# Kernel tuning notes

Measured on AMD Instinct MI355X. Metric: run time of the kernel, lower is better.

## Reference

```python
import jax, jax.numpy as jnp
import numpy as np

# static config (matches init_kwargs)
E = 1280          # n_embed
L = 4             # n_layer
NH = 16           # n_heads
D = E // NH       # head_dim = 80
M = 5120          # n_mlp
O = 2048          # n_output_embed
MS = 2            # spatial_merge_size
NGPS = 48         # sqrt(num_position_embeddings)
GRID_T, GRID_H, GRID_W = 1, 32, 32
N_IMG = 2
SPP = GRID_T * GRID_H * GRID_W   # 1024 tokens per image
S = N_IMG * SPP                  # 2048 total tokens
H4 = E * MS * MS                 # merger hidden = 5120
IN_PATCH = 3 * 2 * 16 * 16       # 1536
DS_IDX = [1, 2]


def _ln(x, w, b, eps=1e-6):
    m = x.mean(-1, keepdims=True)
    v = ((x - m) ** 2).mean(-1, keepdims=True)
    return (x - m) / jnp.sqrt(v + eps) * w + b


def _pos_embed_interp(pos_emb):
    # bilinear interpolation of the 48x48 learned grid to GRID_HxGRID_W, per image
    hi = jnp.linspace(0.0, NGPS - 1.0, GRID_H)
    wi = jnp.linspace(0.0, NGPS - 1.0, GRID_W)
    hf = hi.astype(jnp.int32); wf = wi.astype(jnp.int32)
    hc = jnp.minimum(hf + 1, NGPS - 1); wc = jnp.minimum(wf + 1, NGPS - 1)
    dh = hi - hf; dw = wi - wf
    idx = [(hf[:, None] * NGPS + wf[None]).ravel(), (hf[:, None] * NGPS + wc[None]).ravel(),
           (hc[:, None] * NGPS + wf[None]).ravel(), (hc[:, None] * NGPS + wc[None]).ravel()]
    wts = [((1 - dh)[:, None] * (1 - dw)[None]).ravel(), ((1 - dh)[:, None] * dw[None]).ravel(),
           (dh[:, None] * (1 - dw)[None]).ravel(), (dh[:, None] * dw[None]).ravel()]
    pe = sum(pos_emb[i] * w[:, None] for i, w in zip(idx, wts))  # [h*w, E]
    pe = jnp.tile(pe, (GRID_T, 1))
    # spatial-merge permutation: (t, h/m, m, w/m, m) -> (t, h/m, w/m, m, m)
    pe = pe.reshape(GRID_T, GRID_H // MS, MS, GRID_W // MS, MS, E).transpose(0, 1, 3, 2, 4, 5).reshape(-1, E)
    return jnp.tile(pe, (N_IMG, 1))  # [S, E]


def _rotary_freqs():
    dim = D // 2  # VisionRotaryEmbedding dim = 40
    inv = 1.0 / (10000.0 ** (jnp.arange(0, dim, 2, dtype=jnp.float32) / dim))  # [D//4]
    hp = jnp.broadcast_to(jnp.arange(GRID_H)[:, None], (GRID_H, GRID_W))
    hp = hp.reshape(GRID_H // MS, MS, GRID_W // MS, MS).transpose(0, 2, 1, 3).ravel()
    wp = jnp.broadcast_to(jnp.arange(GRID_W)[None, :], (GRID_H, GRID_W))
    wp = wp.reshape(GRID_H // MS, MS, GRID_W // MS, MS).transpose(0, 2, 1, 3).ravel()
    pos = jnp.stack([hp, wp], -1)            # [h*w, 2]
    pos = jnp.tile(pos, (GRID_T, 1))
    pos = jnp.tile(pos, (N_IMG, 1))          # [S, 2]
    table = jnp.arange(max(GRID_H, GRID_W), dtype=jnp.float32)[:, None] * inv[None]  # [G, D//4]
    return table[pos].reshape(S, -1)         # [S, D//2] (h-freqs || w-freqs)


def _rope(t, cos, sin):
    # t: [S, NH, D]; cos/sin: [S, 1, D]; applied in float32 as in the source
    t1, t2 = jnp.split(t, 2, axis=-1)
    rot = jnp.concatenate([-t2, t1], -1)
    return (t.astype(jnp.float32) * cos + rot.astype(jnp.float32) * sin).astype(t.dtype)


def _attn(x, qkv_w, qkv_b, pw, pb, cos, sin, mask):
    qkv = (x @ qkv_w.T + qkv_b).reshape(S, 3, NH, D)
    q, k, v = qkv[:, 0], qkv[:, 1], qkv[:, 2]
    q = _rope(q, cos, sin)
    k = _rope(k, cos, sin)
    scores = jnp.einsum('shd,thd->hst', q, k) / np.sqrt(D).astype(np.float32) + mask
    p = jax.nn.softmax(scores.astype(jnp.float32), axis=-1).astype(q.dtype)
    o = jnp.einsum('hst,thd->shd', p, v).reshape(S, E)
    return o @ pw.T + pb


def _merger(x, ln_w, ln_b, f1w, f1b, f2w, f2b, post):
    if post:
        x = _ln(x.reshape(-1, H4), ln_w, ln_b)
    else:
        x = _ln(x, ln_w, ln_b).reshape(-1, H4)
    h = jax.nn.gelu(x @ f1w.T + f1b, approximate=False)  # nn.GELU() exact
    return h @ f2w.T + f2b


def setup_inputs() -> dict:
    key = jax.random.key(0)
    ks = iter(jax.random.split(key, 24))
    n = lambda s: jax.random.normal(next(ks), s, dtype=jnp.float32) * 0.02
    return {
        'x': jax.random.normal(next(ks), (S, IN_PATCH), dtype=jnp.float32),
        'patch_w': n((E, IN_PATCH)), 'patch_b': jnp.zeros((E,), jnp.float32),
        'pos_emb': n((NGPS * NGPS, E)),
        'ln1_w': jnp.ones((L, E), jnp.float32), 'ln1_b': jnp.zeros((L, E), jnp.float32),
        'ln2_w': jnp.ones((L, E), jnp.float32), 'ln2_b': jnp.zeros((L, E), jnp.float32),
        'qkv_w': n((L, 3 * E, E)), 'qkv_b': jnp.zeros((L, 3 * E), jnp.float32),
        'attn_proj_w': n((L, E, E)), 'attn_proj_b': jnp.zeros((L, E), jnp.float32),
        'fc1_w': n((L, M, E)), 'fc1_b': jnp.zeros((L, M), jnp.float32),
        'fc2_w': n((L, E, M)), 'fc2_b': jnp.zeros((L, E), jnp.float32),
        'm_ln_w': jnp.ones((E,), jnp.float32), 'm_ln_b': jnp.zeros((E,), jnp.float32),
        'm_fc1_w': n((H4, H4)), 'm_fc1_b': jnp.zeros((H4,), jnp.float32),
        'm_fc2_w': n((O, H4)), 'm_fc2_b': jnp.zeros((O,), jnp.float32),
        'ds_ln_w': jnp.ones((2, H4), jnp.float32), 'ds_ln_b': jnp.zeros((2, H4), jnp.float32),
        'ds_fc1_w': n((2, H4, H4)), 'ds_fc1_b': jnp.zeros((2, H4), jnp.float32),
        'ds_fc2_w': n((2, O, H4)), 'ds_fc2_b': jnp.zeros((2, O), jnp.float32),
    }


def reference(x, patch_w, patch_b, pos_emb, ln1_w, ln1_b, ln2_w, ln2_b,
              qkv_w, qkv_b, attn_proj_w, attn_proj_b, fc1_w, fc1_b, fc2_w, fc2_b,
              m_ln_w, m_ln_b, m_fc1_w, m_fc1_b, m_fc2_w, m_fc2_b,
              ds_ln_w, ds_ln_b, ds_fc1_w, ds_fc1_b, ds_fc2_w, ds_fc2_b):
    # patch embed (Conv3d with kernel==stride == per-patch linear)
    h = x @ patch_w.T + patch_b                      # [S, E]
    h = h + _pos_embed_interp(pos_emb)
    freqs = _rotary_freqs()                          # [S, D//2]
    cos = jnp.concatenate([jnp.cos(freqs)] * 2, -1)[:, None, :]  # [S,1,D]
    sin = jnp.concatenate([jnp.sin(freqs)] * 2, -1)[:, None, :]
    img = jnp.arange(S) // SPP                       # cu_seqlens block-diagonal mask
    mask = jnp.where(img[:, None] == img[None, :], 0.0, jnp.finfo(jnp.float32).min)
    ds_feats = []
    for l in range(L):
        h = h + _attn(_ln(h, ln1_w[l], ln1_b[l]), qkv_w[l], qkv_b[l],
                      attn_proj_w[l], attn_proj_b[l], cos, sin, mask)
        hn = _ln(h, ln2_w[l], ln2_b[l])
        h = h + (jax.nn.gelu(hn @ fc1_w[l].T + fc1_b[l], approximate=True) @ fc2_w[l].T + fc2_b[l])
        if l in DS_IDX:
            j = DS_IDX.index(l)
            ds_feats.append(_merger(h, ds_ln_w[j], ds_ln_b[j], ds_fc1_w[j], ds_fc1_b[j],
                                    ds_fc2_w[j], ds_fc2_b[j], post=True))
    main = _merger(h, m_ln_w, m_ln_b, m_fc1_w, m_fc1_b, m_fc2_w, m_fc2_b, post=False)
    return jnp.stack([main] + ds_feats, 0)           # [3, S//4, O]
```

## Files before the change

kernel.cpp:

```cpp
#include <hip/hip_runtime.h>
#include <hip/hip_bf16.h>
#include <cstdio>
#include <cstdint>

#define E_    1280
#define L_    4
#define NH_   16
#define D_    80
#define DP_   96
#define MLP_  5120
#define O_    2048
#define S_    2048
#define H4_   5120
#define INP_  1536

typedef __attribute__((ext_vector_type(4))) float f32x4;
typedef __attribute__((ext_vector_type(8))) short short8v;
typedef __attribute__((ext_vector_type(4))) short short4v;

__device__ __forceinline__ short f2bf(float f){
  uint32_t u = __float_as_uint(f);
  uint32_t r = (u + 0x7FFFu + ((u >> 16) & 1u)) >> 16;
  return (short)r;
}
__device__ __forceinline__ float bf2f(short s){
  return __uint_as_float(((uint32_t)(uint16_t)s) << 16);
}
__device__ __forceinline__ float gelu_tanh(float x){
  const float z = 0.7978845608028654f*(x + 0.044715f*x*x*x);
  const float e = __expf(2.f*z);
  return 0.5f*x*(1.f + (e-1.f)/(e+1.f));
}
__device__ __forceinline__ float gelu_erf(float x){
  return 0.5f*x*(1.f + erff(x*0.7071067811865476f));
}
__device__ __forceinline__ void token_hw(int t, int& hc, int& wc){
  hc = ((t>>1)&1) + ((t>>6)<<1);
  wc = (t&1)      + (((t>>2)&15)<<1);
}
__device__ __forceinline__ void gload16(const short* g, short* l){
  __builtin_amdgcn_global_load_lds((const __attribute__((address_space(1))) void*)g,
                                   (__attribute__((address_space(3))) void*)l, 16, 0, 0);
}

__global__ __launch_bounds__(256)
void cvt_k(const float* __restrict__ src, short* __restrict__ dst, long long n)
{
  const long long stride = (long long)gridDim.x*256*8;
  for (long long i = ((long long)blockIdx.x*256 + threadIdx.x)*8; i < n; i += stride){
    float4 v0 = *(const float4*)(src+i);
    float4 v1 = *(const float4*)(src+i+4);
    short8v w;
    w[0]=f2bf(v0.x); w[1]=f2bf(v0.y); w[2]=f2bf(v0.z); w[3]=f2bf(v0.w);
    w[4]=f2bf(v1.x); w[5]=f2bf(v1.y); w[6]=f2bf(v1.z); w[7]=f2bf(v1.w);
    *(short8v*)(dst+i) = w;
  }
}

struct Gemm2P {
  const short* A; const short* B; void* C;
  const float* bias;
  short* part;
  int lda, ldb, ldc, M, N, K;
  float scale;
  long long aOffH, aOffI, bOffH, bOffI, cOffH, cOffI;
  int nImg, kSplit;
};

template<int EPI, bool RES, bool CF32, bool SPLIT>
__global__ __launch_bounds__(256)
void gemm2_k(Gemm2P p)
{
  __shared__ short As[3][4096];
  __shared__ short Bs[3][4096];

  int z = blockIdx.z, ks = 0;
  if constexpr (SPLIT){ ks = z % p.kSplit; z /= p.kSplit; }
  const int hI = z / p.nImg, iI = z % p.nImg;
  const long long aB = (long long)hI*p.aOffH + (long long)iI*p.aOffI;
  const long long bB = (long long)hI*p.bOffH + (long long)iI*p.bOffI;
  const long long cB = (long long)hI*p.cOffH + (long long)iI*p.cOffI;

  const int nwg = gridDim.x*gridDim.y;
  const int orig = blockIdx.y*gridDim.x + blockIdx.x;
  const int q8 = nwg >> 3, r8 = nwg & 7;
  const int xcd = orig & 7, oidx = orig >> 3;
  const int wg = (xcd < r8 ? xcd*(q8+1) : r8*(q8+1) + (xcd-r8)*q8) + oidx;
  const int nt = wg % gridDim.x, mt = wg / gridDim.x;

  const int tid = threadIdx.x, lane = tid & 63, wv = tid >> 6;

  const int lam = lane ^ ((lane >> 3) & 7);
  const int sr = lam >> 2;
  const int sc = (lam & 3) * 8;
  const int Kp  = SPLIT ? p.K / p.kSplit : p.K;
  const int kBeg = SPLIT ? ks * Kp : 0;
  const short* pa0 = p.A + aB + (long long)(mt*128 + (wv*2+0)*16 + sr)*p.lda + sc + kBeg;
  const short* pa1 = p.A + aB + (long long)(mt*128 + (wv*2+1)*16 + sr)*p.lda + sc + kBeg;
  const short* pb0 = p.B + bB + (long long)(nt*128 + (wv*2+0)*16 + sr)*p.ldb + sc + kBeg;
  const short* pb1 = p.B + bB + (long long)(nt*128 + (wv*2+1)*16 + sr)*p.ldb + sc + kBeg;
  const int so0 = (wv*2+0)*512;
  const int so1 = (wv*2+1)*512;

  const int fr = lane & 15, g4 = lane >> 4;
  const int wr = (wv >> 1) * 64, wc = (wv & 1) * 64;

  f32x4 acc[4][4] = {};

  auto stage = [&](int buf, int t){
    const int k0 = t << 5;
    gload16(pa0 + k0, &As[buf][so0]);
    gload16(pa1 + k0, &As[buf][so1]);
    gload16(pb0 + k0, &Bs[buf][so0]);
    gload16(pb1 + k0, &Bs[buf][so1]);
  };

  const int ntile = Kp >> 5;
  stage(0, 0);
  if (ntile > 1) stage(1, 1);
  for (int t = 0; t < ntile; t++){
    const int cur = t % 3;
    if (t + 1 < ntile) { asm volatile("s_waitcnt vmcnt(4)" ::: "memory"); }
    else               { asm volatile("s_waitcnt vmcnt(0)" ::: "memory"); }
    __builtin_amdgcn_s_barrier();
    asm volatile("" ::: "memory");
    short8v a[4], b[4];
    #pragma unroll
    for (int i=0;i<4;i++){
      const int ra = wr + i*16 + fr;
      const int ca = (ra*4 + g4) ^ ((ra>>1)&7);
      a[i] = *(const short8v*)&As[cur][ca*8];
      const int rb = wc + i*16 + fr;
      const int cb = (rb*4 + g4) ^ ((rb>>1)&7);
      b[i] = *(const short8v*)&Bs[cur][cb*8];
    }
    if (t + 2 < ntile) stage((t+2)%3, t+2);
    #pragma unroll
    for (int i=0;i<4;i++)
      #pragma unroll
      for (int j=0;j<4;j++)
        acc[i][j] = __builtin_amdgcn_mfma_f32_16x16x32_bf16(a[i], b[j], acc[i][j], 0, 0, 0);
  }

  #pragma unroll
  for (int i=0;i<4;i++){
    #pragma unroll
    for (int j=0;j<4;j++){
      #pragma unroll
      for (int r=0;r<4;r++){
        const int row = mt*128 + wr + i*16 + g4*4 + r;
        const int col = nt*128 + wc + j*16 + fr;
        float v = acc[i][j][r];
        if constexpr (SPLIT){
          p.part[((long long)ks*p.M + row)*p.N + col] = f2bf(v);
        } else {
          if (p.bias) v += p.bias[col];
          if constexpr (EPI==1) v = gelu_tanh(v);
          if constexpr (EPI==2) v = gelu_erf(v);
          if constexpr (EPI==3) v *= p.scale;
          const long long off = cB + (long long)row*p.ldc + col;
          if constexpr (RES)  v += ((const float*)p.C)[off];
          if constexpr (CF32) ((float*)p.C)[off] = v;
          else                ((short*)p.C)[off] = f2bf(v);
        }
      }
    }
  }
}

template<int EPI, bool RES, bool CF32>
__global__ __launch_bounds__(256)
void reduce_k(const short* __restrict__ part, int kSplit, long long MN, int N,
              const float* __restrict__ bias, void* __restrict__ C)
{
  const long long i = ((long long)blockIdx.x*256 + threadIdx.x)*8;
  if (i >= MN) return;
  float v[8];
  { short8v pv = *(const short8v*)(part + i);
    #pragma unroll
    for (int e=0;e<8;e++) v[e] = bf2f(pv[e]); }
  for (int ks = 1; ks < kSplit; ks++){
    short8v pv = *(const short8v*)(part + (long long)ks*MN + i);
    #pragma unroll
    for (int e=0;e<8;e++) v[e] += bf2f(pv[e]);
  }
  if (bias){
    const int col = (int)(i % N);
    #pragma unroll
    for (int e=0;e<8;e++) v[e] += bias[col+e];
  }
  #pragma unroll
  for (int e=0;e<8;e++){
    if constexpr (EPI==1) v[e] = gelu_tanh(v[e]);
    if constexpr (EPI==2) v[e] = gelu_erf(v[e]);
  }
  if constexpr (RES){
    const float* cp = (const float*)C + i;
    #pragma unroll
    for (int e=0;e<8;e++) v[e] += cp[e];
  }
  if constexpr (CF32){
    float4 o0 = {v[0],v[1],v[2],v[3]}, o1 = {v[4],v[5],v[6],v[7]};
    *(float4*)((float*)C + i) = o0;
    *(float4*)((float*)C + i + 4) = o1;
  } else {
    short8v o;
    #pragma unroll
    for (int e=0;e<8;e++) o[e] = f2bf(v[e]);
    *(short8v*)((short*)C + i) = o;
  }
}

__global__ __launch_bounds__(256)
void redln_k(const short* __restrict__ part, long long MN, const float* __restrict__ bias,
             float* __restrict__ h, const float* __restrict__ lnw, const float* __restrict__ lnb,
             short* __restrict__ aln)
{
  __shared__ float red[8];
  const int row = blockIdx.x, tid = threadIdx.x;
  float4 vals[2];
  float s = 0.f, sq = 0.f;
  #pragma unroll
  for (int it=0; it<2; it++){
    const int c = tid*4 + it*1024;
    if (c < E_){
      float4 v = *(const float4*)(h + (long long)row*E_ + c);
      const float4 b = *(const float4*)(bias + c);
      v.x += b.x; v.y += b.y; v.z += b.z; v.w += b.w;
      #pragma unroll
      for (int ks=0; ks<4; ks++){
        short4v pv = *(const short4v*)(part + (long long)ks*MN + (long long)row*E_ + c);
        v.x += bf2f(pv[0]); v.y += bf2f(pv[1]); v.z += bf2f(pv[2]); v.w += bf2f(pv[3]);
      }
      *(float4*)(h + (long long)row*E_ + c) = v;
      vals[it] = v;
      s  += v.x+v.y+v.z+v.w;
      sq += v.x*v.x+v.y*v.y+v.z*v.z+v.w*v.w;
    }
  }
  #pragma unroll
  for (int m=32;m;m>>=1){ s += __shfl_xor(s,m,64); sq += __shfl_xor(sq,m,64); }
  const int wv = tid>>6, lane = tid&63;
  if (lane==0){ red[wv]=s; red[4+wv]=sq; }
  __syncthreads();
  s  = red[0]+red[1]+red[2]+red[3];
  sq = red[4]+red[5]+red[6]+red[7];
  const float mean = s / (float)E_;
  const float var  = sq / (float)E_ - mean*mean;
  const float rs   = rsqrtf(var + 1e-6f);
  #pragma unroll
  for (int it=0; it<2; it++){
    const int c = tid*4 + it*1024;
    if (c < E_){
      const float4 v = vals[it];
      const float4 gw = *(const float4*)(lnw + c);
      const float4 bw = *(const float4*)(lnb + c);
      short4v o;
      o[0] = f2bf((v.x-mean)*rs*gw.x + bw.x);
      o[1] = f2bf((v.y-mean)*rs*gw.y + bw.y);
      o[2] = f2bf((v.z-mean)*rs*gw.z + bw.z);
      o[3] = f2bf((v.w-mean)*rs*gw.w + bw.w);
      *(short4v*)(aln + (long long)row*E_ + c) = o;
    }
  }
}

__global__ __launch_bounds__(256)
void redposln_k(const short* __restrict__ part, long long MN, const float* __restrict__ bias,
                const float* __restrict__ pe, float* __restrict__ h,
                const float* __restrict__ lnw, const float* __restrict__ lnb,
                short* __restrict__ aln)
{
  __shared__ float red[8];
  const int row = blockIdx.x, tid = threadIdx.x;
  const int t = row & 1023;
  int hc, wc; token_hw(t, hc, wc);
  const float hi = (float)hc * (47.f/31.f);
  const float wi = (float)wc * (47.f/31.f);
  int hf = (int)hi; float dh = hi - (float)hf; int h2 = min(hf+1, 47);
  int wf = (int)wi; float dw = wi - (float)wf; int w2 = min(wf+1, 47);
  const float w00=(1.f-dh)*(1.f-dw), w01=(1.f-dh)*dw, w10=dh*(1.f-dw), w11=dh*dw;
  const float* pe00 = pe + (long long)(hf*48+wf)*E_;
  const float* pe01 = pe + (long long)(hf*48+w2)*E_;
  const float* pe10 = pe + (long long)(h2*48+wf)*E_;
  const float* pe11 = pe + (long long)(h2*48+w2)*E_;

  float4 vals[2];
  float s = 0.f, sq = 0.f;
  #pragma unroll
  for (int it=0; it<2; it++){
    const int c = tid*4 + it*1024;
    if (c < E_){
      const float4 b = *(const float4*)(bias + c);
      const float4 a0 = *(const float4*)(pe00 + c);
      const float4 a1 = *(const float4*)(pe01 + c);
      const float4 a2 = *(const float4*)(pe10 + c);
      const float4 a3 = *(const float4*)(pe11 + c);
      float4 v;
      v.x = b.x + w00*a0.x + w01*a1.x + w10*a2.x + w11*a3.x;
      v.y = b.y + w00*a0.y + w01*a1.y + w10*a2.y + w11*a3.y;
      v.z = b.z + w00*a0.z + w01*a1.z + w10*a2.z + w11*a3.z;
      v.w = b.w + w00*a0.w + w01*a1.w + w10*a2.w + w11*a3.w;
      #pragma unroll
      for (int ks=0; ks<4; ks++){
        short4v pv = *(const short4v*)(part + (long long)ks*MN + (long long)row*E_ + c);
        v.x += bf2f(pv[0]); v.y += bf2f(pv[1]); v.z += bf2f(pv[2]); v.w += bf2f(pv[3]);
      }
      *(float4*)(h + (long long)row*E_ + c) = v;
      vals[it] = v;
      s  += v.x+v.y+v.z+v.w;
      sq += v.x*v.x+v.y*v.y+v.z*v.z+v.w*v.w;
    }
  }
  #pragma unroll
  for (int m=32;m;m>>=1){ s += __shfl_xor(s,m,64); sq += __shfl_xor(sq,m,64); }
  const int wv = tid>>6, lane = tid&63;
  if (lane==0){ red[wv]=s; red[4+wv]=sq; }
  __syncthreads();
  s  = red[0]+red[1]+red[2]+red[3];
  sq = red[4]+red[5]+red[6]+red[7];
  const float mean = s / (float)E_;
  const float var  = sq / (float)E_ - mean*mean;
  const float rs   = rsqrtf(var + 1e-6f);
  #pragma unroll
  for (int it=0; it<2; it++){
    const int c = tid*4 + it*1024;
    if (c < E_){
      const float4 v = vals[it];
      const float4 gw = *(const float4*)(lnw + c);
      const float4 bw = *(const float4*)(lnb + c);
      short4v o;
      o[0] = f2bf((v.x-mean)*rs*gw.x + bw.x);
      o[1] = f2bf((v.y-mean)*rs*gw.y + bw.y);
      o[2] = f2bf((v.z-mean)*rs*gw.z + bw.z);
      o[3] = f2bf((v.w-mean)*rs*gw.w + bw.w);
      *(short4v*)(aln + (long long)row*E_ + c) = o;
    }
  }
}

__global__ __launch_bounds__(256)
void fattn_k(const short* __restrict__ qh, const short* __restrict__ kh,
             const short* __restrict__ vt, short* __restrict__ o2)
{
  __shared__ short Ps[4][16*136];

  const int qt = blockIdx.x, h = blockIdx.y, img = blockIdx.z;
  const int tid = threadIdx.x, lane = tid & 63, wv = tid >> 6;
  const int fr = lane & 15, fo = (lane >> 4) * 8, g = lane >> 4;

  const short* qp = qh + ((long long)h*S_ + img*1024 + qt*64 + wv*16)*DP_;
  const short* kp = kh + ((long long)h*S_ + img*1024)*DP_;
  const short* vp = vt + ((long long)(h*2 + img))*80*1024;
  short* Pw = &Ps[wv][0];

  short8v q[3];
  #pragma unroll
  for (int t3=0;t3<3;t3++)
    q[t3] = *(const short8v*)(qp + (long long)fr*DP_ + t3*32 + fo);

  float m_[4], l_[4];
  f32x4 ao[5] = {};
  #pragma unroll
  for (int r=0;r<4;r++){ m_[r] = -3.0e38f; l_[r] = 0.f; }

  const float SC = 0.11180339887498949f * 1.4426950408889634f;

  for (int t = 0; t < 8; t++){
    f32x4 sc[8] = {};
    #pragma unroll
    for (int j=0;j<8;j++){
      #pragma unroll
      for (int t3=0;t3<3;t3++){
        const short8v kb = *(const short8v*)(kp + (long long)(t*128 + j*16 + fr)*DP_ + t3*32 + fo);
        sc[j] = __builtin_amdgcn_mfma_f32_16x16x32_bf16(q[t3], kb, sc[j], 0,0,0);
      }
    }
    #pragma unroll
    for (int j=0;j<8;j++) sc[j] *= SC;

    #pragma unroll
    for (int r=0;r<4;r++){
      float mx = sc[0][r];
      #pragma unroll
      for (int j=1;j<8;j++) mx = fmaxf(mx, sc[j][r]);
      mx = fmaxf(mx, __shfl_xor(mx, 1, 64));
      mx = fmaxf(mx, __shfl_xor(mx, 2, 64));
      mx = fmaxf(mx, __shfl_xor(mx, 4, 64));
      mx = fmaxf(mx, __shfl_xor(mx, 8, 64));
      const float mn = fmaxf(m_[r], mx);
      const float al = exp2f(m_[r] - mn);
      float ts = 0.f;
      #pragma unroll
      for (int j=0;j<8;j++){
        const float pv = exp2f(sc[j][r] - mn);
        sc[j][r] = pv;
        ts += pv;
      }
      ts += __shfl_xor(ts, 1, 64);
      ts += __shfl_xor(ts, 2, 64);
      ts += __shfl_xor(ts, 4, 64);
      ts += __shfl_xor(ts, 8, 64);
      l_[r] = l_[r]*al + ts;
      m_[r] = mn;
      #pragma unroll
      for (int n=0;n<5;n++) ao[n][r] *= al;
      const int prow = g*4 + r;
      #pragma unroll
      for (int j=0;j<8;j++) Pw[prow*136 + j*16 + fr] = f2bf(sc[j][r]);
    }
    asm volatile("s_waitcnt lgkmcnt(0)" ::: "memory");
    __builtin_amdgcn_sched_barrier(0);

    #pragma unroll
    for (int t4=0;t4<4;t4++){
      const short8v pa = *(const short8v*)&Pw[fr*136 + t4*32 + fo];
      #pragma unroll
      for (int n=0;n<5;n++){
        const short8v vb = *(const short8v*)(vp + (long long)(n*16 + fr)*1024 + t*128 + t4*32 + fo);
        ao[n] = __builtin_amdgcn_mfma_f32_16x16x32_bf16(pa, vb, ao[n], 0,0,0);
      }
    }
  }

  short* op = o2 + ((long long)(img*1024 + qt*64 + wv*16))*E_ + h*80;
  #pragma unroll
  for (int r=0;r<4;r++){
    const float inv = 1.f / l_[r];
    const int row = g*4 + r;
    #pragma unroll
    for (int n=0;n<5;n++)
      op[(long long)row*E_ + n*16 + fr] = f2bf(ao[n][r] * inv);
  }
}

__global__ __launch_bounds__(256)
void ln_k(const float* __restrict__ X, const float* __restrict__ g, const float* __restrict__ bta,
          short* __restrict__ Y, int Cn)
{
  __shared__ float red[8];
  const int row = blockIdx.x;
  const float* x = X + (long long)row*Cn;
  short* y = Y + (long long)row*Cn;
  float s = 0.f, sq = 0.f;
  for (int c = threadIdx.x*4; c < Cn; c += 1024){
    float4 v = *(const float4*)(x + c);
    s  += v.x+v.y+v.z+v.w;
    sq += v.x*v.x+v.y*v.y+v.z*v.z+v.w*v.w;
  }
  #pragma unroll
  for (int m=32;m;m>>=1){ s += __shfl_xor(s,m,64); sq += __shfl_xor(sq,m,64); }
  const int wv = threadIdx.x>>6, lane = threadIdx.x&63;
  if (lane==0){ red[wv]=s; red[4+wv]=sq; }
  __syncthreads();
  s  = red[0]+red[1]+red[2]+red[3];
  sq = red[4]+red[5]+red[6]+red[7];
  const float mean = s / (float)Cn;
  const float var  = sq / (float)Cn - mean*mean;
  const float rs   = rsqrtf(var + 1e-6f);
  for (int c = threadIdx.x*4; c < Cn; c += 1024){
    float4 v  = *(const float4*)(x + c);
    float4 gw = *(const float4*)(g + c);
    float4 bw = *(const float4*)(bta + c);
    short4v o;
    o[0] = f2bf((v.x-mean)*rs*gw.x + bw.x);
    o[1] = f2bf((v.y-mean)*rs*gw.y + bw.y);
    o[2] = f2bf((v.z-mean)*rs*gw.z + bw.z);
    o[3] = f2bf((v.w-mean)*rs*gw.w + bw.w);
    *(short4v*)(y + c) = o;
  }
}

__global__ __launch_bounds__(256)
void rope_k(const short* __restrict__ qkv, short* __restrict__ qh,
            short* __restrict__ kh, short* __restrict__ vt)
{
  const int idx = blockIdx.x*256 + threadIdx.x;
  if (idx >= S_*NH_*40) return;
  const int d0 = idx % 40;
  const int h  = (idx / 40) % NH_;
  const int s  = idx / (40*NH_);
  const int t  = s & 1023, img = s >> 10;
  int hc, wc; token_hw(t, hc, wc);
  const int j  = d0 % 20;
  const float invf = exp2f(-0.66438561897747f * (float)j);
  const float pos  = (float)((d0 < 20) ? hc : wc);
  float sn, cs;
  __sincosf(pos * invf, &sn, &cs);
  const short* base = qkv + (long long)s*3840 + h*80;
  const float q1 = bf2f(base[d0]),      q2 = bf2f(base[d0+40]);
  const float k1 = bf2f(base[1280+d0]), k2 = bf2f(base[1280+d0+40]);
  const long long qo = ((long long)h*S_ + s)*DP_;
  qh[qo + d0]    = f2bf(q1*cs - q2*sn);
  qh[qo + d0+40] = f2bf(q2*cs + q1*sn);
  kh[qo + d0]    = f2bf(k1*cs - k2*sn);
  kh[qo + d0+40] = f2bf(k2*cs + k1*sn);
  if (d0 < 16){ qh[qo + 80 + d0] = 0; kh[qo + 80 + d0] = 0; }
  const long long vo = (((long long)h*2 + img)*80)*1024 + t;
  vt[vo + (long long)d0*1024]      = base[2560+d0];
  vt[vo + (long long)(d0+40)*1024] = base[2560+d0+40];
}

static Gemm2P mk(const short* A, const short* B, void* C, const float* bias,
                 int lda, int ldb, int ldc, int M, int N, int K, float scale = 1.f)
{
  Gemm2P p{}; p.A=A; p.B=B; p.C=C; p.bias=bias; p.part=nullptr;
  p.lda=lda; p.ldb=ldb; p.ldc=ldc; p.M=M; p.N=N; p.K=K; p.scale=scale;
  p.aOffH=p.aOffI=p.bOffH=p.bOffI=p.cOffH=p.cOffI=0; p.nImg=1; p.kSplit=1;
  return p;
}

extern "C" void kernel_launch(void* const* d_in, const int* in_sizes, int n_in,
                              void* d_out, int out_size, void* d_ws, size_t ws_size,
                              hipStream_t stream)
{
  const float* x           = (const float*)d_in[0];
  const float* patch_w     = (const float*)d_in[1];
  const float* patch_b     = (const float*)d_in[2];
  const float* pos_emb     = (const float*)d_in[3];
  const float* ln1_w       = (const float*)d_in[4];
  const float* ln1_b       = (const float*)d_in[5];
  const float* ln2_w       = (const float*)d_in[6];
  const float* ln2_b       = (const float*)d_in[7];
  const float* qkv_w       = (const float*)d_in[8];
  const float* qkv_b       = (const float*)d_in[9];
  const float* attn_proj_w = (const float*)d_in[10];
  const float* attn_proj_b = (const float*)d_in[11];
  const float* fc1_w       = (const float*)d_in[12];
  const float* fc1_b       = (const float*)d_in[13];
  const float* fc2_w       = (const float*)d_in[14];
  const float* fc2_b       = (const float*)d_in[15];
  const float* m_ln_w      = (const float*)d_in[16];
  const float* m_ln_b      = (const float*)d_in[17];
  const float* m_fc1_w     = (const float*)d_in[18];
  const float* m_fc1_b     = (const float*)d_in[19];
  const float* m_fc2_w     = (const float*)d_in[20];
  const float* m_fc2_b     = (const float*)d_in[21];
  const float* ds_ln_w     = (const float*)d_in[22];
  const float* ds_ln_b     = (const float*)d_in[23];
  const float* ds_fc1_w    = (const float*)d_in[24];
  const float* ds_fc1_b    = (const float*)d_in[25];
  const float* ds_fc2_w    = (const float*)d_in[26];
  const float* ds_fc2_b    = (const float*)d_in[27];
  float* out = (float*)d_out;

  char* wsp = (char*)d_ws;
  auto alloc = [&](size_t bytes)->char*{
    char* p = wsp; wsp += (bytes + 255) & ~(size_t)255; return p;
  };
  float* h    = (float*)alloc((size_t)S_*E_*4);
  short* qkvb = (short*)alloc((size_t)S_*3840*2);
  short* aln  = (short*)alloc((size_t)S_*E_*2);
  short* qh   = (short*)alloc((size_t)NH_*S_*DP_*2);
  short* kh   = (short*)alloc((size_t)NH_*S_*DP_*2 + 4096);
  short* vt   = (short*)alloc((size_t)NH_*2*D_*1024*2 + 4096);
  short* part = (short*)alloc((size_t)48*1024*1024);
  short* o2   = (short*)alloc((size_t)S_*E_*2);
  short* ffn  = (short*)alloc((size_t)S_*MLP_*2);
  short* xb    = (short*)alloc((size_t)S_*INP_*2);
  short* pwB   = (short*)alloc((size_t)E_*INP_*2);
  short* qkvwB = (short*)alloc((size_t)L_*3840*E_*2);
  short* prwB  = (short*)alloc((size_t)L_*E_*E_*2);
  short* f1wB  = (short*)alloc((size_t)L_*MLP_*E_*2);
  short* f2wB  = (short*)alloc((size_t)L_*E_*MLP_*2);
  short* mf1B  = (short*)alloc((size_t)H4_*H4_*2);
  short* mf2B  = (short*)alloc((size_t)O_*H4_*2);
  short* df1B  = (short*)alloc((size_t)2*H4_*H4_*2);
  short* df2B  = (short*)alloc((size_t)2*O_*H4_*2);
  size_t need = (size_t)(wsp - (char*)d_ws);
  if (need > ws_size){
    fprintf(stderr, "kernel_launch: ws too small: need %zu have %zu\n", need, ws_size);
    return;
  }
  short* dsln = qkvb;

  const dim3 B256(256);
  auto cvt = [&](const float* src, short* dst, long long n){
    unsigned blk = (unsigned)min((long long)8192, (n/8 + 255)/256);
    cvt_k<<<blk, B256, 0, stream>>>(src, dst, n);
  };
  cvt(x, xb, (long long)S_*INP_);
  cvt(patch_w, pwB, (long long)E_*INP_);
  cvt(qkv_w, qkvwB, (long long)L_*3840*E_);
  cvt(attn_proj_w, prwB, (long long)L_*E_*E_);
  cvt(fc1_w, f1wB, (long long)L_*MLP_*E_);
  cvt(fc2_w, f2wB, (long long)L_*E_*MLP_);
  cvt(m_fc1_w, mf1B, (long long)H4_*H4_);
  cvt(m_fc2_w, mf2B, (long long)O_*H4_);
  cvt(ds_fc1_w, df1B, (long long)2*H4_*H4_);
  cvt(ds_fc2_w, df2B, (long long)2*O_*H4_);

  auto G = [](int M, int N, int ks = 1){
    return dim3((unsigned)((N+127)/128), (unsigned)((M+127)/128), (unsigned)ks);
  };
  auto RG = [](long long MN){ return dim3((unsigned)((MN/8 + 255)/256)); };

  { Gemm2P pp = mk(xb, pwB, nullptr, nullptr, INP_, INP_, E_, S_, E_, INP_);
    pp.part = part; pp.kSplit = 4;
    gemm2_k<0,false,true,true><<<G(S_,E_,4),B256,0,stream>>>(pp);
    redposln_k<<<S_, B256, 0, stream>>>(part, (long long)S_*E_, patch_b, pos_emb,
                                        h, ln1_w, ln1_b, aln); }

  for (int l = 0; l < L_; l++){
    { Gemm2P pp = mk(aln, qkvwB + (size_t)l*3840*E_, qkvb, qkv_b + l*3840, E_, E_, 3840, S_, 3840, E_);
      gemm2_k<0,false,false,false><<<G(S_,3840),B256,0,stream>>>(pp); }
    rope_k<<<(S_*NH_*40+255)/256, B256, 0, stream>>>(qkvb, qh, kh, vt);
    fattn_k<<<dim3(16,16,2), B256, 0, stream>>>(qh, kh, vt, o2);
    { Gemm2P pp = mk(o2, prwB + (size_t)l*E_*E_, nullptr, nullptr, E_, E_, E_, S_, E_, E_);
      pp.part = part; pp.kSplit = 4;
      gemm2_k<0,false,true,true><<<G(S_,E_,4),B256,0,stream>>>(pp);
      redln_k<<<S_, B256, 0, stream>>>(part, (long long)S_*E_, attn_proj_b + l*E_,
                                       h, ln2_w + l*E_, ln2_b + l*E_, aln); }

    { Gemm2P pp = mk(aln, f1wB + (size_t)l*MLP_*E_, ffn, fc1_b + l*MLP_, E_, E_, MLP_, S_, MLP_, E_);
      gemm2_k<1,false,false,false><<<G(S_,MLP_),B256,0,stream>>>(pp); }
    { Gemm2P pp = mk(ffn, f2wB + (size_t)l*E_*MLP_, nullptr, nullptr, MLP_, MLP_, E_, S_, E_, MLP_);
      pp.part = part; pp.kSplit = 4;
      gemm2_k<0,false,true,true><<<G(S_,E_,4),B256,0,stream>>>(pp);
      const float* nw = (l < 3) ? (ln1_w + (l+1)*E_) : m_ln_w;
      const float* nb = (l < 3) ? (ln1_b + (l+1)*E_) : m_ln_b;
      redln_k<<<S_, B256, 0, stream>>>(part, (long long)S_*E_, fc2_b + l*E_, h, nw, nb, aln); }

    if (l == 1 || l == 2){
      const int j = l - 1;
      ln_k<<<512, B256, 0, stream>>>(h, ds_ln_w + (size_t)j*H4_, ds_ln_b + (size_t)j*H4_, dsln, H4_);
      { Gemm2P pp = mk(dsln, df1B + (size_t)j*H4_*H4_, ffn, nullptr, H4_, H4_, H4_, 512, H4_, H4_);
        pp.part = part; pp.kSplit = 4;
        gemm2_k<0,false,false,true><<<G(512,H4_,4),B256,0,stream>>>(pp);
        reduce_k<2,false,false><<<RG((long long)512*H4_),B256,0,stream>>>(part, 4, (long long)512*H4_, H4_, ds_fc1_b + (size_t)j*H4_, ffn); }
      { Gemm2P pp = mk(ffn, df2B + (size_t)j*O_*H4_, out + (size_t)(1+j)*512*O_, nullptr, H4_, H4_, O_, 512, O_, H4_);
        pp.part = part; pp.kSplit = 8;
        gemm2_k<0,false,true,true><<<G(512,O_,8),B256,0,stream>>>(pp);
        reduce_k<0,false,true><<<RG((long long)512*O_),B256,0,stream>>>(part, 8, (long long)512*O_, O_, ds_fc2_b + (size_t)j*O_, out + (size_t)(1+j)*512*O_); }
    }
  }

  { Gemm2P pp = mk(aln, mf1B, ffn, nullptr, H4_, H4_, H4_, 512, H4_, H4_);
    pp.part = part; pp.kSplit = 4;
    gemm2_k<0,false,false,true><<<G(512,H4_,4),B256,0,stream>>>(pp);
    reduce_k<2,false,false><<<RG((long long)512*H4_),B256,0,stream>>>(part, 4, (long long)512*H4_, H4_, m_fc1_b, ffn); }
  { Gemm2P pp = mk(ffn, mf2B, out, nullptr, H4_, H4_, O_, 512, O_, H4_);
    pp.part = part; pp.kSplit = 8;
    gemm2_k<0,false,true,true><<<G(512,O_,8),B256,0,stream>>>(pp);
    reduce_k<0,false,true><<<RG((long long)512*O_),B256,0,stream>>>(part, 8, (long long)512*O_, O_, m_fc2_b, out); }
}
```

Baseline: 1.647 ms.

## Fuse fp32-to-bf16 weight conversion into GEMM B-tile loading

Drops the separate conversion kernels that turned every fp32 weight matrix into bf16 before the GEMMs. The GEMM now loads fp32 B tiles into registers, converts them to bf16, and writes them to swizzled LDS one stage ahead, while A still uses direct global-to-LDS loads. This removes a full read and write pass over all weights per call, but doubles the bytes fetched for B inside each GEMM and adds register pressure and conversion ALU work to the main loop. It also removes unused batching and scale fields from the GEMM parameters.

```diff
diff --git a/kernel.cpp b/kernel.cpp
--- a/kernel.cpp
+++ b/kernel.cpp
@@ -58,13 +58,12 @@
 }
 
 struct Gemm2P {
-  const short* A; const short* B; void* C;
+  const short* A; const float* B; void* C;
   const float* bias;
   short* part;
   int lda, ldb, ldc, M, N, K;
   float scale;
-  long long aOffH, aOffI, bOffH, bOffI, cOffH, cOffI;
-  int nImg, kSplit;
+  int kSplit;
 };
 
 template<int EPI, bool RES, bool CF32, bool SPLIT>
@@ -74,12 +73,8 @@
   __shared__ short As[3][4096];
   __shared__ short Bs[3][4096];
 
-  int z = blockIdx.z, ks = 0;
-  if constexpr (SPLIT){ ks = z % p.kSplit; z /= p.kSplit; }
-  const int hI = z / p.nImg, iI = z % p.nImg;
-  const long long aB = (long long)hI*p.aOffH + (long long)iI*p.aOffI;
-  const long long bB = (long long)hI*p.bOffH + (long long)iI*p.bOffI;
-  const long long cB = (long long)hI*p.cOffH + (long long)iI*p.cOffI;
+  int ks = 0;
+  if constexpr (SPLIT){ ks = blockIdx.z; }
 
   const int nwg = gridDim.x*gridDim.y;
   const int orig = blockIdx.y*gridDim.x + blockIdx.x;
@@ -89,39 +84,65 @@
   const int nt = wg % gridDim.x, mt = wg / gridDim.x;
 
   const int tid = threadIdx.x, lane = tid & 63, wv = tid >> 6;
-
-  const int lam = lane ^ ((lane >> 3) & 7);
-  const int sr = lam >> 2;
-  const int sc = (lam & 3) * 8;
   const int Kp  = SPLIT ? p.K / p.kSplit : p.K;
   const int kBeg = SPLIT ? ks * Kp : 0;
-  const short* pa0 = p.A + aB + (long long)(mt*128 + (wv*2+0)*16 + sr)*p.lda + sc + kBeg;
-  const short* pa1 = p.A + aB + (long long)(mt*128 + (wv*2+1)*16 + sr)*p.lda + sc + kBeg;
-  const short* pb0 = p.B + bB + (long long)(nt*128 + (wv*2+0)*16 + sr)*p.ldb + sc + kBeg;
-  const short* pb1 = p.B + bB + (long long)(nt*128 + (wv*2+1)*16 + sr)*p.ldb + sc + kBeg;
+
+  const int lam = lane ^ ((lane >> 3) & 7);
+  const int asr = lam >> 2, asc = (lam & 3) * 8;
+  const short* pa0 = p.A + (long long)(mt*128 + (wv*2+0)*16 + asr)*p.lda + asc + kBeg;
+  const short* pa1 = p.A + (long long)(mt*128 + (wv*2+1)*16 + asr)*p.lda + asc + kBeg;
   const int so0 = (wv*2+0)*512;
   const int so1 = (wv*2+1)*512;
 
+  const int bsr = lane >> 2, bcc = lane & 3;
+  const int brow0 = (wv*2+0)*16 + bsr, brow1 = (wv*2+1)*16 + bsr;
+  const float* pbf0 = p.B + (long long)(nt*128 + brow0)*p.ldb + bcc*8 + kBeg;
+  const float* pbf1 = p.B + (long long)(nt*128 + brow1)*p.ldb + bcc*8 + kBeg;
+  const int wch0 = ((brow0*4 + bcc) ^ ((brow0>>1)&7)) * 8;
+  const int wch1 = ((brow1*4 + bcc) ^ ((brow1>>1)&7)) * 8;
+
   const int fr = lane & 15, g4 = lane >> 4;
   const int wr = (wv >> 1) * 64, wc = (wv & 1) * 64;
 
   f32x4 acc[4][4] = {};
-
-  auto stage = [&](int buf, int t){
+  float4 br0, br1, br2, br3;
+
+  auto loadB = [&](int t){
+    const int k0 = t << 5;
+    br0 = *(const float4*)(pbf0 + k0);
+    br1 = *(const float4*)(pbf0 + k0 + 4);
+    br2 = *(const float4*)(pbf1 + k0);
+    br3 = *(const float4*)(pbf1 + k0 + 4);
+  };
+  auto stageA = [&](int buf, int t){
     const int k0 = t << 5;
     gload16(pa0 + k0, &As[buf][so0]);
     gload16(pa1 + k0, &As[buf][so1]);
-    gload16(pb0 + k0, &Bs[buf][so0]);
-    gload16(pb1 + k0, &Bs[buf][so1]);
   };
+  auto writeB = [&](int buf){
+    short8v w0, w1;
+    w0[0]=f2bf(br0.x); w0[1]=f2bf(br0.y); w0[2]=f2bf(br0.z); w0[3]=f2bf(br0.w);
+    w0[4]=f2bf(br1.x); w0[5]=f2bf(br1.y); w0[6]=f2bf(br1.z); w0[7]=f2bf(br1.w);
+    w1[0]=f2bf(br2.x); w1[1]=f2bf(br2.y); w1[2]=f2bf(br2.z); w1[3]=f2bf(br2.w);
+    w1[4]=f2bf(br3.x); w1[5]=f2bf(br3.y); w1[6]=f2bf(br3.z); w1[7]=f2bf(br3.w);
+    *(short8v*)&Bs[buf][wch0] = w0;
+    *(short8v*)&Bs[buf][wch1] = w1;
+  };
 
   const int ntile = Kp >> 5;
-  stage(0, 0);
-  if (ntile > 1) stage(1, 1);
+  loadB(0);
+  stageA(0, 0);
+  asm volatile("s_waitcnt vmcnt(2)" ::: "memory");
+  writeB(0);
+  if (ntile > 1){ loadB(1); stageA(1, 1); }
+
   for (int t = 0; t < ntile; t++){
     const int cur = t % 3;
-    if (t + 1 < ntile) { asm volatile("s_waitcnt vmcnt(4)" ::: "memory"); }
+    if (t + 1 < ntile) { asm volatile("s_waitcnt vmcnt(2)" ::: "memory"); }
     else               { asm volatile("s_waitcnt vmcnt(0)" ::: "memory"); }
+    if (t + 1 < ntile) writeB((t+1) % 3);
+    if (t + 2 < ntile) loadB(t+2);
+    asm volatile("s_waitcnt lgkmcnt(0)" ::: "memory");
     __builtin_amdgcn_s_barrier();
     asm volatile("" ::: "memory");
     short8v a[4], b[4];
@@ -134,7 +155,7 @@
       const int cb = (rb*4 + g4) ^ ((rb>>1)&7);
       b[i] = *(const short8v*)&Bs[cur][cb*8];
     }
-    if (t + 2 < ntile) stage((t+2)%3, t+2);
+    if (t + 2 < ntile) stageA((t+2)%3, t+2);
     #pragma unroll
     for (int i=0;i<4;i++)
       #pragma unroll
@@ -157,8 +178,7 @@
           if (p.bias) v += p.bias[col];
           if constexpr (EPI==1) v = gelu_tanh(v);
           if constexpr (EPI==2) v = gelu_erf(v);
-          if constexpr (EPI==3) v *= p.scale;
-          const long long off = cB + (long long)row*p.ldc + col;
+          const long long off = (long long)row*p.ldc + col;
           if constexpr (RES)  v += ((const float*)p.C)[off];
           if constexpr (CF32) ((float*)p.C)[off] = v;
           else                ((short*)p.C)[off] = f2bf(v);
@@ -501,12 +521,11 @@
   vt[vo + (long long)(d0+40)*1024] = base[2560+d0+40];
 }
 
-static Gemm2P mk(const short* A, const short* B, void* C, const float* bias,
-                 int lda, int ldb, int ldc, int M, int N, int K, float scale = 1.f)
+static Gemm2P mk(const short* A, const float* B, void* C, const float* bias,
+                 int lda, int ldb, int ldc, int M, int N, int K)
 {
   Gemm2P p{}; p.A=A; p.B=B; p.C=C; p.bias=bias; p.part=nullptr;
-  p.lda=lda; p.ldb=ldb; p.ldc=ldc; p.M=M; p.N=N; p.K=K; p.scale=scale;
-  p.aOffH=p.aOffI=p.bOffH=p.bOffI=p.cOffH=p.cOffI=0; p.nImg=1; p.kSplit=1;
+  p.lda=lda; p.ldb=ldb; p.ldc=ldc; p.M=M; p.N=N; p.K=K; p.scale=1.f; p.kSplit=1;
   return p;
 }
 
@@ -557,16 +576,7 @@
   short* part = (short*)alloc((size_t)48*1024*1024);
   short* o2   = (short*)alloc((size_t)S_*E_*2);
   short* ffn  = (short*)alloc((size_t)S_*MLP_*2);
-  short* xb    = (short*)alloc((size_t)S_*INP_*2);
-  short* pwB   = (short*)alloc((size_t)E_*INP_*2);
-  short* qkvwB = (short*)alloc((size_t)L_*3840*E_*2);
-  short* prwB  = (short*)alloc((size_t)L_*E_*E_*2);
-  short* f1wB  = (short*)alloc((size_t)L_*MLP_*E_*2);
-  short* f2wB  = (short*)alloc((size_t)L_*E_*MLP_*2);
-  short* mf1B  = (short*)alloc((size_t)H4_*H4_*2);
-  short* mf2B  = (short*)alloc((size_t)O_*H4_*2);
-  short* df1B  = (short*)alloc((size_t)2*H4_*H4_*2);
-  short* df2B  = (short*)alloc((size_t)2*O_*H4_*2);
+  short* xb   = (short*)alloc((size_t)S_*INP_*2);
   size_t need = (size_t)(wsp - (char*)d_ws);
   if (need > ws_size){
     fprintf(stderr, "kernel_launch: ws too small: need %zu have %zu\n", need, ws_size);
@@ -575,46 +585,35 @@
   short* dsln = qkvb;
 
   const dim3 B256(256);
-  auto cvt = [&](const float* src, short* dst, long long n){
+  { long long n = (long long)S_*INP_;
     unsigned blk = (unsigned)min((long long)8192, (n/8 + 255)/256);
-    cvt_k<<<blk, B256, 0, stream>>>(src, dst, n);
-  };
-  cvt(x, xb, (long long)S_*INP_);
-  cvt(patch_w, pwB, (long long)E_*INP_);
-  cvt(qkv_w, qkvwB, (long long)L_*3840*E_);
-  cvt(attn_proj_w, prwB, (long long)L_*E_*E_);
-  cvt(fc1_w, f1wB, (long long)L_*MLP_*E_);
-  cvt(fc2_w, f2wB, (long long)L_*E_*MLP_);
-  cvt(m_fc1_w, mf1B, (long long)H4_*H4_);
-  cvt(m_fc2_w, mf2B, (long long)O_*H4_);
-  cvt(ds_fc1_w, df1B, (long long)2*H4_*H4_);
-  cvt(ds_fc2_w, df2B, (long long)2*O_*H4_);
+    cvt_k<<<blk, B256, 0, stream>>>(x, xb, n); }
 
   auto G = [](int M, int N, int ks = 1){
     return dim3((unsigned)((N+127)/128), (unsigned)((M+127)/128), (unsigned)ks);
   };
   auto RG = [](long long MN){ return dim3((unsigned)((MN/8 + 255)/256)); };
 
-  { Gemm2P pp = mk(xb, pwB, nullptr, nullptr, INP_, INP_, E_, S_, E_, INP_);
+  { Gemm2P pp = mk(xb, patch_w, nullptr, nullptr, INP_, INP_, E_, S_, E_, INP_);
     pp.part = part; pp.kSplit = 4;
     gemm2_k<0,false,true,true><<<G(S_,E_,4),B256,0,stream>>>(pp);
     redposln_k<<<S_, B256, 0, stream>>>(part, (long long)S_*E_, patch_b, pos_emb,
                                         h, ln1_w, ln1_b, aln); }
 
   for (int l = 0; l < L_; l++){
-    { Gemm2P pp = mk(aln, qkvwB + (size_t)l*3840*E_, qkvb, qkv_b + l*3840, E_, E_, 3840, S_, 3840, E_);
+    { Gemm2P pp = mk(aln, qkv_w + (size_t)l*3840*E_, qkvb, qkv_b + l*3840, E_, E_, 3840, S_, 3840, E_);
       gemm2_k<0,false,false,false><<<G(S_,3840),B256,0,stream>>>(pp); }
     rope_k<<<(S_*NH_*40+255)/256, B256, 0, stream>>>(qkvb, qh, kh, vt);
     fattn_k<<<dim3(16,16,2), B256, 0, stream>>>(qh, kh, vt, o2);
-    { Gemm2P pp = mk(o2, prwB + (size_t)l*E_*E_, nullptr, nullptr, E_, E_, E_, S_, E_, E_);
+    { Gemm2P pp = mk(o2, attn_proj_w + (size_t)l*E_*E_, nullptr, nullptr, E_, E_, E_, S_, E_, E_);
       pp.part = part; pp.kSplit = 4;
       gemm2_k<0,false,true,true><<<G(S_,E_,4),B256,0,stream>>>(pp);
       redln_k<<<S_, B256, 0, stream>>>(part, (long long)S_*E_, attn_proj_b + l*E_,
                                        h, ln2_w + l*E_, ln2_b + l*E_, aln); }
 
-    { Gemm2P pp = mk(aln, f1wB + (size_t)l*MLP_*E_, ffn, fc1_b + l*MLP_, E_, E_, MLP_, S_, MLP_, E_);
+    { Gemm2P pp = mk(aln, fc1_w + (size_t)l*MLP_*E_, ffn, fc1_b + l*MLP_, E_, E_, MLP_, S_, MLP_, E_);
       gemm2_k<1,false,false,false><<<G(S_,MLP_),B256,0,stream>>>(pp); }
-    { Gemm2P pp = mk(ffn, f2wB + (size_t)l*E_*MLP_, nullptr, nullptr, MLP_, MLP_, E_, S_, E_, MLP_);
+    { Gemm2P pp = mk(ffn, fc2_w + (size_t)l*E_*MLP_, nullptr, nullptr, MLP_, MLP_, E_, S_, E_, MLP_);
       pp.part = part; pp.kSplit = 4;
       gemm2_k<0,false,true,true><<<G(S_,E_,4),B256,0,stream>>>(pp);
       const float* nw = (l < 3) ? (ln1_w + (l+1)*E_) : m_ln_w;
@@ -624,22 +623,22 @@
     if (l == 1 || l == 2){
       const int j = l - 1;
       ln_k<<<512, B256, 0, stream>>>(h, ds_ln_w + (size_t)j*H4_, ds_ln_b + (size_t)j*H4_, dsln, H4_);
-      { Gemm2P pp = mk(dsln, df1B + (size_t)j*H4_*H4_, ffn, nullptr, H4_, H4_, H4_, 512, H4_, H4_);
+      { Gemm2P pp = mk(dsln, ds_fc1_w + (size_t)j*H4_*H4_, ffn, nullptr, H4_, H4_, H4_, 512, H4_, H4_);
         pp.part = part; pp.kSplit = 4;
         gemm2_k<0,false,false,true><<<G(512,H4_,4),B256,0,stream>>>(pp);
         reduce_k<2,false,false><<<RG((long long)512*H4_),B256,0,stream>>>(part, 4, (long long)512*H4_, H4_, ds_fc1_b + (size_t)j*H4_, ffn); }
-      { Gemm2P pp = mk(ffn, df2B + (size_t)j*O_*H4_, out + (size_t)(1+j)*512*O_, nullptr, H4_, H4_, O_, 512, O_, H4_);
+      { Gemm2P pp = mk(ffn, ds_fc2_w + (size_t)j*O_*H4_, out + (size_t)(1+j)*512*O_, nullptr, H4_, H4_, O_, 512, O_, H4_);
         pp.part = part; pp.kSplit = 8;
         gemm2_k<0,false,true,true><<<G(512,O_,8),B256,0,stream>>>(pp);
         reduce_k<0,false,true><<<RG((long long)512*O_),B256,0,stream>>>(part, 8, (long long)512*O_, O_, ds_fc2_b + (size_t)j*O_, out + (size_t)(1+j)*512*O_); }
     }
   }
 
-  { Gemm2P pp = mk(aln, mf1B, ffn, nullptr, H4_, H4_, H4_, 512, H4_, H4_);
+  { Gemm2P pp = mk(aln, m_fc1_w, ffn, nullptr, H4_, H4_, H4_, 512, H4_, H4_);
     pp.part = part; pp.kSplit = 4;
     gemm2_k<0,false,false,true><<<G(512,H4_,4),B256,0,stream>>>(pp);
     reduce_k<2,false,false><<<RG((long long)512*H4_),B256,0,stream>>>(part, 4, (long long)512*H4_, H4_, m_fc1_b, ffn); }
-  { Gemm2P pp = mk(ffn, mf2B, out, nullptr, H4_, H4_, O_, 512, O_, H4_);
+  { Gemm2P pp = mk(ffn, m_fc2_w, out, nullptr, H4_, H4_, O_, 512, O_, H4_);
     pp.part = part; pp.kSplit = 8;
     gemm2_k<0,false,true,true><<<G(512,O_,8),B256,0,stream>>>(pp);
     reduce_k<0,false,true><<<RG((long long)512*O_),B256,0,stream>>>(part, 8, (long long)512*O_, O_, m_fc2_b, out); }
```

New measurement: 1.763 ms. 1.07x slower.
